# Kernel optimization log

Hardware: AMD Instinct MI355X
Metric: run time of the kernel (lower is better)

## Reference

```python
import jax, jax.numpy as jnp
import numpy as np

D_MODEL = 1024; D_STATE = 64; D_CONV = 7; EXPAND = 2; HEADDIM = 64; NGROUPS = 1
D_INNER = EXPAND * D_MODEL            # 2048
NHEADS = D_INNER // HEADDIM           # 32
D_IN_PROJ = 2 * D_INNER + 2 * (2 * NGROUPS * D_STATE) + 2 * NHEADS  # 4416
CONV_DIM = D_INNER + 2 * (2 * NGROUPS * D_STATE)                     # 2304
BATCH = 2; SEQLEN = 2048
EPS = 1e-5


def setup_inputs() -> dict:
    key = jax.random.key(0)
    ks = jax.random.split(key, 8)
    u = jax.random.normal(ks[0], (BATCH, SEQLEN, D_MODEL), jnp.float32)
    W_in = jax.random.normal(ks[1], (D_IN_PROJ, D_MODEL), jnp.float32) * 0.02
    conv_w = jax.random.normal(ks[2], (CONV_DIM, 1, D_CONV), jnp.float32) * 0.2
    conv_b = jax.random.normal(ks[3], (CONV_DIM,), jnp.float32) * 0.02
    # dt_bias init as in module: inv-softplus of dt sampled log-uniform in [dt_min, dt_max]
    dt = jnp.exp(jax.random.uniform(ks[4], (NHEADS,)) * (np.log(0.1) - np.log(0.001)) + np.log(0.001))
    dt = jnp.clip(dt, 1e-4)
    dt_bias = dt + jnp.log(-jnp.expm1(-dt))
    A_log = jnp.zeros((NHEADS,), jnp.float32)          # A = -exp(A_log) = -1
    Dp = jnp.ones((NHEADS,), jnp.float32)
    fc_D_w = jax.random.normal(ks[5], (NHEADS, D_INNER), jnp.float32) * 0.02
    norm_w = jnp.ones((D_INNER,), jnp.float32)
    W_out = jax.random.normal(ks[6], (D_MODEL, D_INNER), jnp.float32) * 0.02
    return dict(u=u, W_in=W_in, conv_w=conv_w, conv_b=conv_b, dt_bias=dt_bias,
                A_log=A_log, Dp=Dp, fc_D_w=fc_D_w, norm_w=norm_w, W_out=W_out)


def reference(u, W_in, conv_w, conv_b, dt_bias, A_log, Dp, fc_D_w, norm_w, W_out):
    b, L, _ = u.shape
    gn = NGROUPS * D_STATE
    zxbcdt = jnp.einsum('bld,ed->ble', u, W_in)              # (b,L,4416)
    A = -jnp.exp(A_log)                                       # (H,)
    z = zxbcdt[..., :D_INNER]
    xBC = zxbcdt[..., D_INNER:D_INNER + CONV_DIM]
    dt_raw = zxbcdt[..., D_INNER + CONV_DIM:]                 # (b,L,2H)
    # fwd dt + time-flipped bwd dt stacked along batch -> (2b,L,H)
    dt = jnp.concatenate([dt_raw[..., :NHEADS], dt_raw[..., NHEADS:][:, ::-1]], axis=0)
    dt = jax.nn.softplus(dt + dt_bias)                        # dt_limit=(0,inf): softplus already >= 0
    # depthwise conv1d, 'same' padding
    xc = jnp.transpose(xBC, (0, 2, 1))                        # (b,Cd,L)
    xc = jax.lax.conv_general_dilated(xc, conv_w, (1,), [(D_CONV // 2, D_CONV // 2)],
                                      dimension_numbers=('NCH', 'OIH', 'NCH'),
                                      feature_group_count=CONV_DIM)
    xc = xc + conv_b[None, :, None]
    xBC = jax.nn.silu(jnp.transpose(xc, (0, 2, 1)))           # (b,L,Cd)
    x = xBC[..., :D_INNER]
    BC = xBC[..., D_INNER:]
    x_og = x
    x2 = jnp.concatenate([x, x[:, ::-1]], axis=0)             # (2b,L,d_inner)
    BC2 = jnp.concatenate([BC[..., :2 * gn], BC[..., 2 * gn:][:, ::-1]], axis=0)
    Bm = BC2[..., :gn].reshape(2 * b, L, NGROUPS, D_STATE)
    Cm = BC2[..., gn:].reshape(2 * b, L, NGROUPS, D_STATE)
    x_scan = x2.reshape(2 * b, L, NHEADS, HEADDIM)
    hpg = NHEADS // NGROUPS
    Bh = jnp.repeat(Bm, hpg, axis=2)                          # (2b,L,H,N)
    Ch = jnp.repeat(Cm, hpg, axis=2)

    def step(state, ins):                                     # state: (2b,H,P,N)
        x_t, dt_t, B_t, C_t = ins
        ex = jnp.exp(A[None, :, None, None] * dt_t[:, :, None, None])
        state = state * ex + x_t[..., None] * B_t[:, :, None, :]
        y_t = jnp.sum(state * C_t[:, :, None, :], axis=-1)    # (2b,H,P)
        return state, y_t

    xs = (jnp.moveaxis(x_scan, 1, 0), jnp.moveaxis(dt, 1, 0),
          jnp.moveaxis(Bh, 1, 0), jnp.moveaxis(Ch, 1, 0))
    state0 = jnp.zeros((2 * b, NHEADS, HEADDIM, D_STATE), u.dtype)
    _, ys = jax.lax.scan(step, state0, xs)                    # (L,2b,H,P)
    y = jnp.moveaxis(ys, 0, 1).reshape(2 * b, L, D_INNER)
    # shift_right: drop last step, zero at t=0
    y = jnp.concatenate([jnp.zeros_like(y[:, :1]), y[:, :-1]], axis=1)
    y_fw, y_bw = y[:b], y[b:][:, ::-1]
    diag_heads = jnp.einsum('bld,hd->blh', x_og, fc_D_w) + Dp # fc_D(x_og) with bias D
    diag = jnp.repeat(diag_heads, HEADDIM, axis=-1)           # expand per-head -> d_inner
    y = y_fw + y_bw + x_og * diag
    # RMSNormGated (norm before gate)
    rms = jnp.sqrt(jnp.mean(y * y, axis=-1, keepdims=True) + EPS)
    y = norm_w * (y / rms) * jax.nn.silu(z)
    return jnp.einsum('ble,de->bld', y, W_out)
```

## Files before the change

kernel.cpp:

```cpp
#include <hip/hip_runtime.h>
#include <cstdint>
#include <cstddef>

#define L_SEQ   2048
#define DMODEL  1024
#define DINNER  2048
#define NHEADS_ 32
#define HEADDIM_ 64
#define DSTATE  64
#define CONVDIM 2304
#define DINPROJ 4416
#define DINPROJ_P 4480
#define BATCH_  2
#define EPS_    1e-5f
#define PITCH   72
#define KSPL    8

typedef __attribute__((ext_vector_type(8))) short bf16x8;
typedef __attribute__((ext_vector_type(4))) float f32x4;
typedef unsigned short ushort_t;
typedef unsigned int uint_t;
typedef __attribute__((address_space(3))) unsigned int as3_uint;
typedef __attribute__((address_space(1))) const unsigned int as1_uint;

__device__ __forceinline__ float silu_f(float v) { return v / (1.f + __expf(-v)); }
__device__ __forceinline__ ushort_t f2bf(float f) {
    uint_t u = __float_as_uint(f);
    return (ushort_t)((u + 0x7FFFu + ((u >> 16) & 1u)) >> 16);
}
__device__ __forceinline__ float bf2f(ushort_t u) {
    return __uint_as_float(((uint_t)u) << 16);
}
__device__ __forceinline__ void gload16(const void* g, void* l) {
    __builtin_amdgcn_global_load_lds((as1_uint*)g, (as3_uint*)l, 16, 0, 0);
}

#define N0U ((size_t)(4096 * 1024 / 4))
#define N1U ((size_t)(DINPROJ_P * DMODEL / 4))
#define N2U ((size_t)(DMODEL * DINNER / 4))
#define N3U ((size_t)(64 * DINNER / 4))
__global__ __launch_bounds__(256)
void cvt_all(const float* __restrict__ u, const float* __restrict__ W_in,
             const float* __restrict__ W_out, const float* __restrict__ fcD,
             ushort_t* __restrict__ ubf, ushort_t* __restrict__ wibf,
             ushort_t* __restrict__ wobf, ushort_t* __restrict__ fcdbf) {
    size_t unit = (size_t)blockIdx.x * 256 + threadIdx.x;
    const float* src; ushort_t* dst; size_t i4; bool zero = false;
    if (unit < N0U) {
        i4 = unit; src = u; dst = ubf;
    } else if (unit < N0U + N1U) {
        i4 = unit - N0U; src = W_in; dst = wibf;
        zero = ((int)(i4 / (DMODEL / 4)) >= DINPROJ);
    } else if (unit < N0U + N1U + N2U) {
        i4 = unit - N0U - N1U; src = W_out; dst = wobf;
    } else {
        i4 = unit - N0U - N1U - N2U; src = fcD; dst = fcdbf;
        zero = ((int)(i4 / (DINNER / 4)) >= NHEADS_);
    }
    float4 v = zero ? make_float4(0.f, 0.f, 0.f, 0.f)
                    : reinterpret_cast<const float4*>(src)[i4];
    ushort_t* d = dst + i4 * 4;
    d[0] = f2bf(v.x); d[1] = f2bf(v.y); d[2] = f2bf(v.z); d[3] = f2bf(v.w);
}

template<int BM, int BN, int WGM, int WGN, int FM, int FN, int MODE>
__global__ __launch_bounds__(256)
void gemm_nt_mfma(const ushort_t* __restrict__ A, const ushort_t* __restrict__ B,
                  float* __restrict__ C, ushort_t* __restrict__ Cbf,
                  int M, int N, int K, int lda, int ldb, int nbn) {
    const int nwg = gridDim.x;
    const int orig = blockIdx.x;
    const int xcd = orig & 7, q = nwg >> 3, r = nwg & 7;
    const int wg = ((xcd < r) ? (xcd * (q + 1)) : (r * (q + 1) + (xcd - r) * q)) + (orig >> 3);

    int bm, bn, kbeg, kend, ks = 0;
    if (MODE == 2) {
        bm = (wg / nbn) * BM; bn = 0; ks = wg % nbn;
        kbeg = ks * (K / nbn); kend = kbeg + K / nbn;
    } else {
        bm = (wg / nbn) * BM; bn = (wg % nbn) * BN;
        kbeg = 0; kend = K;
    }

    constexpr int BUFSZ = (BM + BN) * 64;
    constexpr int EPI_B = (MODE == 2) ? 0 : BM * 256;
    constexpr int SMEM_B = (2 * BUFSZ > EPI_B) ? 2 * BUFSZ : EPI_B;
    __shared__ __align__(16) char smem[SMEM_B];

    const int tid = threadIdx.x;
    const int wave = tid >> 6, lane = tid & 63;
    const int wr = wave / WGN, wc = wave % WGN;
    const int fr = lane & 15, kg = lane >> 4;

    constexpr int AI = BM / 64, BI = BN / 64;
    size_t aoff[AI]; int aLds[AI];
#pragma unroll
    for (int pp = 0; pp < AI; ++pp) {
        int p = wave * AI + pp;
        int row = p * 16 + (lane >> 2);
        int c16 = (lane & 3) ^ ((row >> 1) & 3);
        aoff[pp] = (size_t)(bm + row) * lda + c16 * 8;
        aLds[pp] = p * 1024;
    }
    size_t boff[BI]; int bLds[BI];
#pragma unroll
    for (int pp = 0; pp < BI; ++pp) {
        int p = wave * BI + pp;
        int row = p * 16 + (lane >> 2);
        int c16 = (lane & 3) ^ ((row >> 1) & 3);
        boff[pp] = (size_t)(bn + row) * ldb + c16 * 8;
        bLds[pp] = BM * 64 + p * 1024;
    }

    auto stage = [&](int buf, int k0) {
        char* bp = smem + buf * BUFSZ;
#pragma unroll
        for (int pp = 0; pp < AI; ++pp) gload16(&A[aoff[pp] + k0], bp + aLds[pp]);
#pragma unroll
        for (int pp = 0; pp < BI; ++pp) gload16(&B[boff[pp] + k0], bp + bLds[pp]);
    };

    f32x4 acc[FM][FN];
#pragma unroll
    for (int m = 0; m < FM; ++m)
#pragma unroll
        for (int n = 0; n < FN; ++n) acc[m][n] = (f32x4){0.f, 0.f, 0.f, 0.f};

    stage(0, kbeg);
    __syncthreads();

    const int NT = (kend - kbeg) / 32;
    for (int t = 0; t < NT; ++t) {
        const int cur = t & 1;
        if (t + 1 < NT) stage(cur ^ 1, kbeg + (t + 1) * 32);

        const char* bp = smem + cur * BUFSZ;
        bf16x8 af[FM], bfv[FN];
#pragma unroll
        for (int m = 0; m < FM; ++m) {
            int row = wr * FM * 16 + m * 16 + fr;
            af[m] = *reinterpret_cast<const bf16x8*>(bp + row * 64 + ((kg ^ ((row >> 1) & 3)) << 4));
        }
#pragma unroll
        for (int n = 0; n < FN; ++n) {
            int row = wc * FN * 16 + n * 16 + fr;
            bfv[n] = *reinterpret_cast<const bf16x8*>(bp + BM * 64 + row * 64 + ((kg ^ ((row >> 1) & 3)) << 4));
        }
#pragma unroll
        for (int m = 0; m < FM; ++m)
#pragma unroll
            for (int n = 0; n < FN; ++n)
                acc[m][n] = __builtin_amdgcn_mfma_f32_16x16x32_bf16(af[m], bfv[n], acc[m][n], 0, 0, 0);
        __syncthreads();
    }

    const int rg = lane >> 4;
    if (MODE == 2) {
        float* Cp = C + (size_t)ks * M * NHEADS_;
#pragma unroll
        for (int m = 0; m < FM; ++m)
#pragma unroll
            for (int n = 0; n < FN; ++n) {
                int col = wc * FN * 16 + n * 16 + fr;
#pragma unroll
                for (int r = 0; r < 4; ++r) {
                    int rowg = bm + wr * FM * 16 + m * 16 + rg * 4 + r;
                    if (col < NHEADS_) Cp[(size_t)rowg * NHEADS_ + col] = acc[m][n][r];
                }
            }
    } else {
        constexpr int ESZ = (MODE == 1) ? 2 : 4;
        char* ct = smem;
#pragma unroll
        for (int m = 0; m < FM; ++m)
#pragma unroll
            for (int n = 0; n < FN; ++n) {
#pragma unroll
                for (int r = 0; r < 4; ++r) {
                    int lr = wr * FM * 16 + m * 16 + rg * 4 + r;
                    int lc = wc * FN * 16 + n * 16 + fr;
                    int byte = (lr * 256 + lc * ESZ) ^ ((lr & 7) << 4);
                    if (MODE == 1) *reinterpret_cast<ushort_t*>(ct + byte) = f2bf(acc[m][n][r]);
                    else           *reinterpret_cast<float*>(ct + byte) = acc[m][n][r];
                }
            }
        __syncthreads();
        const int lrow = tid >> 4, seg16 = (tid & 15) * 16;
#pragma unroll
        for (int j = 0; j < BM / 16; ++j) {
            int lr = j * 16 + lrow;
            uint4 v = *reinterpret_cast<const uint4*>(ct + ((lr * 256 + seg16) ^ ((lr & 7) << 4)));
            if (MODE == 1)
                *reinterpret_cast<uint4*>(&Cbf[(size_t)(bm + lr) * N + bn + seg16 / 2]) = v;
            else
                *reinterpret_cast<uint4*>(&C[(size_t)(bm + lr) * N + bn + seg16 / 4]) = v;
        }
    }
}

__global__ __launch_bounds__(256)
void conv_kernel(const ushort_t* __restrict__ zxbf, const float* __restrict__ conv_w,
                 const float* __restrict__ conv_b, ushort_t* __restrict__ xBCbf) {
    const int c = blockIdx.x * 256 + threadIdx.x;
    const int t0 = blockIdx.y * 16;
    const int beta = blockIdx.z;
    float w[7];
#pragma unroll
    for (int k = 0; k < 7; ++k) w[k] = conv_w[c * 7 + k];
    const float bias = conv_b[c];
    const ushort_t* in = zxbf + (size_t)beta * L_SEQ * DINPROJ_P + DINNER + c;
    float win[7];
#pragma unroll
    for (int j = 0; j < 6; ++j) {
        int t = t0 - 3 + j;
        win[j] = (t >= 0 && t < L_SEQ) ? bf2f(in[(size_t)t * DINPROJ_P]) : 0.f;
    }
    for (int i = 0; i < 16; ++i) {
        int t = t0 + i;
        int tl = t + 3;
        win[6] = (tl < L_SEQ) ? bf2f(in[(size_t)tl * DINPROJ_P]) : 0.f;
        float acc = bias;
#pragma unroll
        for (int k = 0; k < 7; ++k) acc += win[k] * w[k];
        xBCbf[((size_t)beta * L_SEQ + t) * CONVDIM + c] = f2bf(silu_f(acc));
#pragma unroll
        for (int j = 0; j < 6; ++j) win[j] = win[j + 1];
    }
}

__global__ __launch_bounds__(256)
void dtla_kernel(const ushort_t* __restrict__ zxbf, const float* __restrict__ dt_bias,
                 const float* __restrict__ A_log, float* __restrict__ labuf) {
    const int idx = blockIdx.x * 256 + threadIdx.x;
    const int h   = idx & 31;
    const int tau = (idx >> 5) & (L_SEQ - 1);
    const int bd  = idx >> 16;
    const int dir = bd >> 1, beta = bd & 1;
    const int tt  = dir ? (L_SEQ - 1 - tau) : tau;
    const float dtraw = bf2f(zxbf[((size_t)beta * L_SEQ + tt) * DINPROJ_P + DINNER + CONVDIM + dir * NHEADS_ + h]);
    const float Ah = -__expf(A_log[h]);
    const float dtv = dtraw + dt_bias[h];
    const float sp = (dtv > 15.f) ? dtv : log1pf(__expf(dtv));
    labuf[((size_t)bd * NHEADS_ + h) * L_SEQ + tau] = Ah * sp;
}

__global__ __launch_bounds__(256)
void ssd_chunk_kernel(const ushort_t* __restrict__ xBCbf, const float* __restrict__ labuf,
                      float* __restrict__ Pbuf, ushort_t* __restrict__ sdel,
                      ushort_t* __restrict__ yfw, ushort_t* __restrict__ ybw) {
    const int c  = blockIdx.x;
    const int h  = blockIdx.y;
    const int bd = blockIdx.z;
    const int dir = bd >> 1, beta = bd & 1;
    const int tid = threadIdx.x;
    const int wave = tid >> 6, lane = tid & 63;
    const int wr = wave >> 1, wc = wave & 1;
    const int fr = lane & 15, kg = lane >> 4, rg = lane >> 4;

    __shared__ short Bs[64 * PITCH], Cs[64 * PITCH], XTs[64 * PITCH],
                     BTs[64 * PITCH], Ms[64 * PITCH];
    __shared__ float lslds[64];

    const int row = tid >> 2, seg = tid & 3;
    const int tau_r = c * 64 + row;
    const int tt = dir ? (L_SEQ - 1 - tau_r) : tau_r;
    const ushort_t* gbase = xBCbf + ((size_t)beta * L_SEQ + tt) * CONVDIM;

    union U4 { uint4 v; ushort_t s[8]; };
    U4 x0, x1, b0, b1, c0, c1;
    x0.v = *reinterpret_cast<const uint4*>(gbase + h * 64 + seg * 16);
    x1.v = *reinterpret_cast<const uint4*>(gbase + h * 64 + seg * 16 + 8);
    b0.v = *reinterpret_cast<const uint4*>(gbase + DINNER + dir * 128 + seg * 16);
    b1.v = *reinterpret_cast<const uint4*>(gbase + DINNER + dir * 128 + seg * 16 + 8);
    c0.v = *reinterpret_cast<const uint4*>(gbase + DINNER + dir * 128 + 64 + seg * 16);
    c1.v = *reinterpret_cast<const uint4*>(gbase + DINNER + dir * 128 + 64 + seg * 16 + 8);

    *reinterpret_cast<uint4*>(&Bs[row * PITCH + seg * 16])     = b0.v;
    *reinterpret_cast<uint4*>(&Bs[row * PITCH + seg * 16 + 8]) = b1.v;
    *reinterpret_cast<uint4*>(&Cs[row * PITCH + seg * 16])     = c0.v;
    *reinterpret_cast<uint4*>(&Cs[row * PITCH + seg * 16 + 8]) = c1.v;
#pragma unroll
    for (int k = 0; k < 8; ++k) {
        XTs[(seg * 16 + k) * PITCH + row]     = x0.s[k];
        XTs[(seg * 16 + 8 + k) * PITCH + row] = x1.s[k];
    }

    if (tid < 64) {
        float v = labuf[((size_t)bd * NHEADS_ + h) * L_SEQ + c * 64 + tid];
#pragma unroll
        for (int d = 1; d < 64; d <<= 1) {
            float t = __shfl_up(v, d);
            if (lane >= d) v += t;
        }
        lslds[tid] = v;
        Pbuf[((size_t)bd * NHEADS_ + h) * L_SEQ + c * 64 + tid] = __expf(v);
    }
    __syncthreads();

    {
        const float wrow = __expf(lslds[63] - lslds[row]);
#pragma unroll
        for (int k = 0; k < 8; ++k) {
            BTs[(seg * 16 + k) * PITCH + row]     = (short)f2bf(bf2f(b0.s[k]) * wrow);
            BTs[(seg * 16 + 8 + k) * PITCH + row] = (short)f2bf(bf2f(b1.s[k]) * wrow);
        }
    }

    f32x4 accg[2][2];
#pragma unroll
    for (int mi = 0; mi < 2; ++mi)
#pragma unroll
        for (int nj = 0; nj < 2; ++nj) accg[mi][nj] = (f32x4){0.f, 0.f, 0.f, 0.f};
#pragma unroll
    for (int s = 0; s < 2; ++s) {
        int koff = kg * 8 + s * 32;
        bf16x8 af[2], bfv[2];
#pragma unroll
        for (int mi = 0; mi < 2; ++mi)
            af[mi] = *reinterpret_cast<const bf16x8*>(&Cs[(wr * 32 + mi * 16 + fr) * PITCH + koff]);
#pragma unroll
        for (int nj = 0; nj < 2; ++nj)
            bfv[nj] = *reinterpret_cast<const bf16x8*>(&Bs[(wc * 32 + nj * 16 + fr) * PITCH + koff]);
#pragma unroll
        for (int mi = 0; mi < 2; ++mi)
#pragma unroll
            for (int nj = 0; nj < 2; ++nj)
                accg[mi][nj] = __builtin_amdgcn_mfma_f32_16x16x32_bf16(af[mi], bfv[nj], accg[mi][nj], 0, 0, 0);
    }

#pragma unroll
    for (int mi = 0; mi < 2; ++mi)
#pragma unroll
        for (int nj = 0; nj < 2; ++nj) {
            int j = wc * 32 + nj * 16 + fr;
            float lsj = lslds[j];
#pragma unroll
            for (int r = 0; r < 4; ++r) {
                int i = wr * 32 + mi * 16 + rg * 4 + r;
                float v = accg[mi][nj][r];
                v = (i >= j) ? v * __expf(lslds[i] - lsj) : 0.f;
                Ms[i * PITCH + j] = (short)f2bf(v);
            }
        }
    __syncthreads();

    f32x4 accy[2][2], accs[2][2];
#pragma unroll
    for (int mi = 0; mi < 2; ++mi)
#pragma unroll
        for (int nj = 0; nj < 2; ++nj) {
            accy[mi][nj] = (f32x4){0.f, 0.f, 0.f, 0.f};
            accs[mi][nj] = (f32x4){0.f, 0.f, 0.f, 0.f};
        }
#pragma unroll
    for (int s = 0; s < 2; ++s) {
        int koff = kg * 8 + s * 32;
        bf16x8 am[2], axt[2], bxt[2], bbt[2];
#pragma unroll
        for (int mi = 0; mi < 2; ++mi) {
            am[mi]  = *reinterpret_cast<const bf16x8*>(&Ms[(wr * 32 + mi * 16 + fr) * PITCH + koff]);
            axt[mi] = *reinterpret_cast<const bf16x8*>(&XTs[(wr * 32 + mi * 16 + fr) * PITCH + koff]);
        }
#pragma unroll
        for (int nj = 0; nj < 2; ++nj) {
            bxt[nj] = *reinterpret_cast<const bf16x8*>(&XTs[(wc * 32 + nj * 16 + fr) * PITCH + koff]);
            bbt[nj] = *reinterpret_cast<const bf16x8*>(&BTs[(wc * 32 + nj * 16 + fr) * PITCH + koff]);
        }
#pragma unroll
        for (int mi = 0; mi < 2; ++mi)
#pragma unroll
            for (int nj = 0; nj < 2; ++nj) {
                accy[mi][nj] = __builtin_amdgcn_mfma_f32_16x16x32_bf16(am[mi], bxt[nj], accy[mi][nj], 0, 0, 0);
                accs[mi][nj] = __builtin_amdgcn_mfma_f32_16x16x32_bf16(axt[mi], bbt[nj], accs[mi][nj], 0, 0, 0);
            }
    }

    ushort_t* Yt = (ushort_t*)Bs;
    ushort_t* St = (ushort_t*)Cs;
#pragma unroll
    for (int mi = 0; mi < 2; ++mi)
#pragma unroll
        for (int nj = 0; nj < 2; ++nj) {
#pragma unroll
            for (int r = 0; r < 4; ++r) {
                int i  = wr * 32 + mi * 16 + rg * 4 + r;
                int jd = wc * 32 + nj * 16 + fr;
                St[i * 64 + jd] = f2bf(accs[mi][nj][r]);
                Yt[i * 64 + jd] = f2bf(accy[mi][nj][r]);
            }
        }
    __syncthreads();

    ushort_t* yout = dir ? ybw : yfw;
    ushort_t* sdp = sdel + (((size_t)bd * NHEADS_ + h) * 32 + c) * 4096;
    for (int un = tid; un < 512; un += 256) {
        const int rowi = un >> 3, ch = un & 7;
        uint4 sv = *reinterpret_cast<const uint4*>(St + rowi * 64 + ch * 8);
        *reinterpret_cast<uint4*>(sdp + rowi * 64 + ch * 8) = sv;
        uint4 yv = *reinterpret_cast<const uint4*>(Yt + rowi * 64 + ch * 8);
        int tau = c * 64 + rowi;
        int tout;
        if (tau == L_SEQ - 1) { tout = dir ? (L_SEQ - 1) : 0; yv = make_uint4(0, 0, 0, 0); }
        else                  { tout = dir ? (L_SEQ - 2 - tau) : (tau + 1); }
        *reinterpret_cast<uint4*>(yout + ((size_t)beta * L_SEQ + tout) * DINNER + h * 64 + ch * 8) = yv;
    }
}

__global__ __launch_bounds__(256)
void ssd_scan_kernel(const float* __restrict__ Pbuf, ushort_t* __restrict__ sdel) {
    const int bh = blockIdx.x;
    const int qt = blockIdx.y;
    const int eo = qt * 1024 + threadIdx.x * 4;
    ushort_t* base = sdel + (size_t)bh * 32 * 4096;
    const float* Pb = Pbuf + (size_t)bh * L_SEQ;

    float S0 = 0.f, S1 = 0.f, S2 = 0.f, S3 = 0.f;
    uint2 d = *reinterpret_cast<const uint2*>(base + eo);
    for (int c = 0; c < 32; ++c) {
        uint2 dn;
        if (c + 1 < 32) dn = *reinterpret_cast<const uint2*>(base + (size_t)(c + 1) * 4096 + eo);
        const float ptot = Pb[c * 64 + 63];
        uint2 pv;
        pv.x = (uint_t)f2bf(S0) | ((uint_t)f2bf(S1) << 16);
        pv.y = (uint_t)f2bf(S2) | ((uint_t)f2bf(S3) << 16);
        *reinterpret_cast<uint2*>(base + (size_t)c * 4096 + eo) = pv;
        S0 = ptot * S0 + bf2f((ushort_t)(d.x & 0xFFFF));
        S1 = ptot * S1 + bf2f((ushort_t)(d.x >> 16));
        S2 = ptot * S2 + bf2f((ushort_t)(d.y & 0xFFFF));
        S3 = ptot * S3 + bf2f((ushort_t)(d.y >> 16));
        d = dn;
    }
}

__global__ __launch_bounds__(256)
void ssd_yinter_kernel(const ushort_t* __restrict__ xBCbf, const float* __restrict__ Pbuf,
                       const ushort_t* __restrict__ sin_buf,
                       ushort_t* __restrict__ yfw, ushort_t* __restrict__ ybw) {
    const int c  = blockIdx.x;
    const int h  = blockIdx.y;
    const int bd = blockIdx.z;
    const int dir = bd >> 1, beta = bd & 1;
    const int tid = threadIdx.x;
    const int wave = tid >> 6, lane = tid & 63;
    const int fr = lane & 15, kg = lane >> 4, rg = lane >> 4;
    const int i0 = wave * 16;

    __shared__ short Cs[64 * PITCH], Ss[64 * PITCH];
    __shared__ float Pl[64];

    const int row = tid >> 2, seg = tid & 3;
    {
        const int tau_r = c * 64 + row;
        const int tt = dir ? (L_SEQ - 1 - tau_r) : tau_r;
        const ushort_t* gbase = xBCbf + ((size_t)beta * L_SEQ + tt) * CONVDIM + DINNER + dir * 128 + 64;
        uint4 cv0 = *reinterpret_cast<const uint4*>(gbase + seg * 16);
        uint4 cv1 = *reinterpret_cast<const uint4*>(gbase + seg * 16 + 8);
        *reinterpret_cast<uint4*>(&Cs[row * PITCH + seg * 16])     = cv0;
        *reinterpret_cast<uint4*>(&Cs[row * PITCH + seg * 16 + 8]) = cv1;
    }
    {
        const ushort_t* sb = sin_buf + (((size_t)bd * NHEADS_ + h) * 32 + c) * 4096;
        for (int un = tid; un < 512; un += 256) {
            const int ri = un >> 3, ch = un & 7;
            uint4 v = *reinterpret_cast<const uint4*>(sb + ri * 64 + ch * 8);
            *reinterpret_cast<uint4*>(&Ss[ri * PITCH + ch * 8]) = v;
        }
    }
    if (tid < 64) Pl[tid] = Pbuf[((size_t)bd * NHEADS_ + h) * L_SEQ + c * 64 + tid];
    __syncthreads();

    f32x4 accy[4];
#pragma unroll
    for (int nf = 0; nf < 4; ++nf) accy[nf] = (f32x4){0.f, 0.f, 0.f, 0.f};
#pragma unroll
    for (int s = 0; s < 2; ++s) {
        int koff = kg * 8 + s * 32;
        bf16x8 af = *reinterpret_cast<const bf16x8*>(&Cs[(i0 + fr) * PITCH + koff]);
#pragma unroll
        for (int nf = 0; nf < 4; ++nf) {
            bf16x8 bfv = *reinterpret_cast<const bf16x8*>(&Ss[(nf * 16 + fr) * PITCH + koff]);
            accy[nf] = __builtin_amdgcn_mfma_f32_16x16x32_bf16(af, bfv, accy[nf], 0, 0, 0);
        }
    }
    __syncthreads();

    ushort_t* Yt = (ushort_t*)Cs;
#pragma unroll
    for (int nf = 0; nf < 4; ++nf) {
        int hdl = nf * 16 + fr;
#pragma unroll
        for (int r = 0; r < 4; ++r) {
            int i = i0 + rg * 4 + r;
            Yt[i * 64 + hdl] = f2bf(accy[nf][r] * Pl[i]);
        }
    }
    __syncthreads();

    ushort_t* yout = dir ? ybw : yfw;
    for (int un = tid; un < 512; un += 256) {
        const int ri = un >> 3, ch = un & 7;
        int tau = c * 64 + ri;
        if (tau == L_SEQ - 1) continue;
        int tout = dir ? (L_SEQ - 2 - tau) : (tau + 1);
        ushort_t* gp = yout + ((size_t)beta * L_SEQ + tout) * DINNER + h * 64 + ch * 8;
        union U4 { uint4 v; ushort_t s[8]; } yo, cv, res;
        yo.v = *reinterpret_cast<const uint4*>(gp);
        cv.v = *reinterpret_cast<const uint4*>(Yt + ri * 64 + ch * 8);
#pragma unroll
        for (int k = 0; k < 8; ++k) res.s[k] = f2bf(bf2f(yo.s[k]) + bf2f(cv.s[k]));
        *reinterpret_cast<uint4*>(gp) = res.v;
    }
}

__global__ __launch_bounds__(256)
void combine_rms(const ushort_t* __restrict__ yfw, const ushort_t* __restrict__ ybw,
                 const ushort_t* __restrict__ xBCbf, const float* __restrict__ dpart,
                 const float* __restrict__ Dp,
                 const ushort_t* __restrict__ zxbf, const float* __restrict__ norm_w,
                 ushort_t* __restrict__ ybf) {
    const int row = blockIdx.x;
    const int tid = threadIdx.x;
    union U4 { uint4 v; ushort_t s[8]; };
    U4 yf, yb, xv, zv;
    yf.v = *reinterpret_cast<const uint4*>(yfw + (size_t)row * DINNER + tid * 8);
    yb.v = *reinterpret_cast<const uint4*>(ybw + (size_t)row * DINNER + tid * 8);
    xv.v = *reinterpret_cast<const uint4*>(xBCbf + (size_t)row * CONVDIM + tid * 8);
    zv.v = *reinterpret_cast<const uint4*>(zxbf + (size_t)row * DINPROJ_P + tid * 8);
    const int hh = tid >> 3;
    float dgv = Dp[hh];
#pragma unroll
    for (int ks = 0; ks < KSPL; ++ks)
        dgv += dpart[((size_t)ks * (BATCH_ * L_SEQ) + row) * NHEADS_ + hh];
    float v[8];
    float ss = 0.f;
#pragma unroll
    for (int i = 0; i < 8; ++i) {
        float val = bf2f(yf.s[i]) + bf2f(yb.s[i]) + bf2f(xv.s[i]) * dgv;
        v[i] = val;
        ss += val * val;
    }
    ss += __shfl_xor(ss, 1);  ss += __shfl_xor(ss, 2);  ss += __shfl_xor(ss, 4);
    ss += __shfl_xor(ss, 8);  ss += __shfl_xor(ss, 16); ss += __shfl_xor(ss, 32);
    __shared__ float wsum[4];
    if ((tid & 63) == 0) wsum[tid >> 6] = ss;
    __syncthreads();
    ss = wsum[0] + wsum[1] + wsum[2] + wsum[3];
    const float inv = rsqrtf(ss * (1.f / DINNER) + EPS_);
    U4 outv;
#pragma unroll
    for (int i = 0; i < 8; ++i) {
        int c = tid * 8 + i;
        outv.s[i] = f2bf(norm_w[c] * v[i] * inv * silu_f(bf2f(zv.s[i])));
    }
    *reinterpret_cast<uint4*>(ybf + (size_t)row * DINNER + tid * 8) = outv.v;
}

extern "C" void kernel_launch(void* const* d_in, const int* in_sizes, int n_in,
                              void* d_out, int out_size, void* d_ws, size_t ws_size,
                              hipStream_t stream) {
    const float* u       = (const float*)d_in[0];
    const float* W_in    = (const float*)d_in[1];
    const float* conv_w  = (const float*)d_in[2];
    const float* conv_b  = (const float*)d_in[3];
    const float* dt_bias = (const float*)d_in[4];
    const float* A_log   = (const float*)d_in[5];
    const float* Dp      = (const float*)d_in[6];
    const float* fc_D_w  = (const float*)d_in[7];
    const float* norm_w  = (const float*)d_in[8];
    const float* W_out   = (const float*)d_in[9];
    float* out = (float*)d_out;

    const int ROWS = BATCH_ * L_SEQ;
    ushort_t* zxbf  = (ushort_t*)d_ws;
    ushort_t* xBCbf = zxbf  + (size_t)ROWS * DINPROJ_P;
    ushort_t* yfw   = xBCbf + (size_t)ROWS * CONVDIM;
    ushort_t* ybw   = yfw   + (size_t)ROWS * DINNER;
    float* dpart = (float*)(ybw + (size_t)ROWS * DINNER);
    float* labuf = dpart + (size_t)KSPL * ROWS * NHEADS_;
    float* Pbuf  = labuf + (size_t)4 * NHEADS_ * L_SEQ;
    ushort_t* sdel = (ushort_t*)(Pbuf + (size_t)4 * NHEADS_ * L_SEQ);
    ushort_t* wobf = sdel + (size_t)4 * NHEADS_ * 32 * 64 * 64;
    ushort_t* fcdbf = wobf + (size_t)DMODEL * DINNER;
    ushort_t* ubf  = fcdbf + (size_t)64 * DINNER;
    ushort_t* wibf = ubf  + (size_t)ROWS * DMODEL;
    ushort_t* ybf  = ubf;

    const size_t total_units = N0U + N1U + N2U + N3U;
    cvt_all<<<(int)((total_units + 255) / 256), 256, 0, stream>>>(
        u, W_in, W_out, fc_D_w, ubf, wibf, wobf, fcdbf);

    gemm_nt_mfma<128, 128, 2, 2, 4, 4, 1><<<(ROWS / 128) * (DINPROJ_P / 128), 256, 0, stream>>>(
        ubf, wibf, nullptr, zxbf, ROWS, DINPROJ_P, DMODEL, DMODEL, DMODEL, DINPROJ_P / 128);

    dim3 gc(CONVDIM / 256, L_SEQ / 16, BATCH_);
    conv_kernel<<<gc, 256, 0, stream>>>(zxbf, conv_w, conv_b, xBCbf);

    dtla_kernel<<<(4 * L_SEQ * NHEADS_) / 256, 256, 0, stream>>>(zxbf, dt_bias, A_log, labuf);

    dim3 ga(32, NHEADS_, 4);
    ssd_chunk_kernel<<<ga, 256, 0, stream>>>(xBCbf, labuf, Pbuf, sdel, yfw, ybw);

    dim3 gsn(4 * NHEADS_, 4);
    ssd_scan_kernel<<<gsn, 256, 0, stream>>>(Pbuf, sdel);

    dim3 gy(32, NHEADS_, 4);
    ssd_yinter_kernel<<<gy, 256, 0, stream>>>(xBCbf, Pbuf, sdel, yfw, ybw);

    gemm_nt_mfma<64, 64, 2, 2, 2, 2, 2><<<(ROWS / 64) * KSPL, 256, 0, stream>>>(
        xBCbf, fcdbf, dpart, nullptr, ROWS, 64, DINNER, CONVDIM, DINNER, KSPL);

    combine_rms<<<ROWS, 256, 0, stream>>>(yfw, ybw, xBCbf, dpart, Dp, zxbf, norm_w, ybf);

    gemm_nt_mfma<128, 64, 2, 2, 4, 2, 0><<<(ROWS / 128) * (DMODEL / 64), 256, 0, stream>>>(
        ybf, wobf, out, nullptr, ROWS, DMODEL, DINNER, DINNER, DINNER, DMODEL / 64);
}
```

Measured before the change: 207.3 us.

## Replace in-projection GEMM with 256x256-tile 8-wave phased MFMA kernel

Measured after the change: 219.6 us. +5.9%, slower.

```diff
diff --git a/kernel.cpp b/kernel.cpp
--- a/kernel.cpp
+++ b/kernel.cpp
@@ -10,7 +10,7 @@
 #define DSTATE  64
 #define CONVDIM 2304
 #define DINPROJ 4416
-#define DINPROJ_P 4480
+#define DINPROJ_P 4608
 #define BATCH_  2
 #define EPS_    1e-5f
 #define PITCH   72
@@ -45,6 +45,7 @@
              ushort_t* __restrict__ ubf, ushort_t* __restrict__ wibf,
              ushort_t* __restrict__ wobf, ushort_t* __restrict__ fcdbf) {
     size_t unit = (size_t)blockIdx.x * 256 + threadIdx.x;
+    if (unit >= N0U + N1U + N2U + N3U) return;
     const float* src; ushort_t* dst; size_t i4; bool zero = false;
     if (unit < N0U) {
         i4 = unit; src = u; dst = ubf;
@@ -63,6 +64,137 @@
     d[0] = f2bf(v.x); d[1] = f2bf(v.y); d[2] = f2bf(v.z); d[3] = f2bf(v.w);
 }
 
+__global__ __launch_bounds__(512, 2)
+void gemm_8ph(const ushort_t* __restrict__ Ap, const ushort_t* __restrict__ Bp,
+              ushort_t* __restrict__ Cbf, int M, int N, int K, int nbn) {
+    const int nwg = gridDim.x;
+    const int orig = blockIdx.x;
+    const int xcd = orig & 7, q_ = nwg >> 3, r_ = nwg & 7;
+    const int wg = ((xcd < r_) ? (xcd * (q_ + 1)) : (r_ * (q_ + 1) + (xcd - r_) * q_)) + (orig >> 3);
+    const int bm = (wg / nbn) * 256, bn = (wg % nbn) * 256;
+
+    __shared__ __align__(16) char smem[131072];
+
+    const int tid = threadIdx.x;
+    const int wave = tid >> 6, lane = tid & 63;
+    const int wr = wave >> 2, wc = wave & 3;
+    const int fr = lane & 15, kg = lane >> 4, rg = lane >> 4;
+
+    const ushort_t* gptr[8]; uint_t glds[8];
+#pragma unroll
+    for (int i = 0; i < 8; ++i) {
+        int unit = i >> 1, g = i & 1;
+        int isB = unit & 1, half = unit >> 1;
+        int rbase = half * 128 + wave * 16 + g * 8;
+        int rl = rbase + (lane >> 3);
+        int slot = (lane & 7) ^ (lane >> 3);
+        gptr[i] = (isB ? Bp : Ap) + (size_t)((isB ? bn : bm) + rl) * (size_t)K + slot * 8;
+        glds[i] = (uint_t)(isB * 32768 + rbase * 128);
+    }
+    auto stage = [&](int pbuf, int t) {
+#pragma unroll
+        for (int i = 0; i < 8; ++i)
+            gload16(gptr[i] + (size_t)t * 64, smem + pbuf * 65536 + glds[i]);
+    };
+
+    f32x4 acc[8][4];
+#pragma unroll
+    for (int m = 0; m < 8; ++m)
+#pragma unroll
+        for (int n = 0; n < 4; ++n) acc[m][n] = (f32x4){0.f, 0.f, 0.f, 0.f};
+
+    bf16x8 aF[4][2];
+    bf16x8 bF[2][2][2];
+
+    auto lda_frag = [&](int pbuf, int mh) {
+#pragma unroll
+        for (int mm = 0; mm < 4; ++mm)
+#pragma unroll
+            for (int kk = 0; kk < 2; ++kk) {
+                int Rl = wr * 128 + mh * 64 + mm * 16 + fr;
+                aF[mm][kk] = *reinterpret_cast<const bf16x8*>(
+                    smem + pbuf * 65536 + Rl * 128 + (((kk * 4 + kg) ^ (Rl & 7)) << 4));
+            }
+    };
+    auto ldb_frag = [&](int pbuf, int nh) {
+#pragma unroll
+        for (int nn = 0; nn < 2; ++nn)
+#pragma unroll
+            for (int kk = 0; kk < 2; ++kk) {
+                int Rl = wc * 64 + (nh * 2 + nn) * 16 + fr;
+                bF[nh][nn][kk] = *reinterpret_cast<const bf16x8*>(
+                    smem + pbuf * 65536 + 32768 + Rl * 128 + (((kk * 4 + kg) ^ (Rl & 7)) << 4));
+            }
+    };
+    auto do_mfma = [&](int mh, int nh) {
+        __builtin_amdgcn_s_setprio(1);
+#pragma unroll
+        for (int mm = 0; mm < 4; ++mm)
+#pragma unroll
+            for (int nn = 0; nn < 2; ++nn)
+#pragma unroll
+                for (int kk = 0; kk < 2; ++kk)
+                    acc[mh * 4 + mm][nh * 2 + nn] = __builtin_amdgcn_mfma_f32_16x16x32_bf16(
+                        aF[mm][kk], bF[nh][nn][kk], acc[mh * 4 + mm][nh * 2 + nn], 0, 0, 0);
+        __builtin_amdgcn_s_setprio(0);
+    };
+
+    const int NT = K / 64;
+    stage(0, 0);
+    asm volatile("s_waitcnt vmcnt(0)" ::: "memory");
+    __builtin_amdgcn_sched_barrier(0);
+    __builtin_amdgcn_s_barrier();
+
+    for (int t = 0; t < NT; ++t) {
+        const int p = t & 1;
+        if (t + 1 < NT) stage(p ^ 1, t + 1);
+        if (t > 0) {
+            if (t + 1 < NT) asm volatile("s_waitcnt vmcnt(8)" ::: "memory");
+            else            asm volatile("s_waitcnt vmcnt(0)" ::: "memory");
+            __builtin_amdgcn_sched_barrier(0);
+        }
+        __builtin_amdgcn_s_barrier();
+        lda_frag(p, 0); ldb_frag(p, 0);
+        asm volatile("s_waitcnt lgkmcnt(0)" ::: "memory");
+        __builtin_amdgcn_sched_barrier(0);
+        do_mfma(0, 0);
+        __builtin_amdgcn_s_barrier();
+        ldb_frag(p, 1);
+        asm volatile("s_waitcnt lgkmcnt(0)" ::: "memory");
+        __builtin_amdgcn_sched_barrier(0);
+        do_mfma(0, 1);
+        __builtin_amdgcn_s_barrier();
+        lda_frag(p, 1);
+        asm volatile("s_waitcnt lgkmcnt(0)" ::: "memory");
+        __builtin_amdgcn_sched_barrier(0);
+        do_mfma(1, 0);
+        __builtin_amdgcn_s_barrier();
+        do_mfma(1, 1);
+        __builtin_amdgcn_s_barrier();
+    }
+
+    char* ct = smem;
+#pragma unroll
+    for (int m = 0; m < 8; ++m)
+#pragma unroll
+        for (int n = 0; n < 4; ++n) {
+#pragma unroll
+            for (int r = 0; r < 4; ++r) {
+                int lr = wr * 128 + m * 16 + rg * 4 + r;
+                int lc = wc * 64 + n * 16 + fr;
+                int byte = lr * 512 + ((lc * 2) ^ ((lr & 7) << 4));
+                *reinterpret_cast<ushort_t*>(ct + byte) = f2bf(acc[m][n][r]);
+            }
+        }
+    __syncthreads();
+    for (int pass = 0; pass < 16; ++pass) {
+        int unit = pass * 512 + tid;
+        int row = unit >> 5, u = unit & 31;
+        uint4 v = *reinterpret_cast<const uint4*>(ct + row * 512 + ((u * 16) ^ ((row & 7) << 4)));
+        *reinterpret_cast<uint4*>(&Cbf[(size_t)(bm + row) * N + bn + u * 8]) = v;
+    }
+}
+
 template<int BM, int BN, int WGM, int WGN, int FM, int FN, int MODE>
 __global__ __launch_bounds__(256)
 void gemm_nt_mfma(const ushort_t* __restrict__ A, const ushort_t* __restrict__ B,
@@ -169,7 +301,6 @@
                 }
             }
     } else {
-        constexpr int ESZ = (MODE == 1) ? 2 : 4;
         char* ct = smem;
 #pragma unroll
         for (int m = 0; m < FM; ++m)
@@ -179,9 +310,8 @@
                 for (int r = 0; r < 4; ++r) {
                     int lr = wr * FM * 16 + m * 16 + rg * 4 + r;
                     int lc = wc * FN * 16 + n * 16 + fr;
-                    int byte = (lr * 256 + lc * ESZ) ^ ((lr & 7) << 4);
-                    if (MODE == 1) *reinterpret_cast<ushort_t*>(ct + byte) = f2bf(acc[m][n][r]);
-                    else           *reinterpret_cast<float*>(ct + byte) = acc[m][n][r];
+                    int byte = (lr * 256 + lc * 4) ^ ((lr & 7) << 4);
+                    *reinterpret_cast<float*>(ct + byte) = acc[m][n][r];
                 }
             }
         __syncthreads();
@@ -190,10 +320,7 @@
         for (int j = 0; j < BM / 16; ++j) {
             int lr = j * 16 + lrow;
             uint4 v = *reinterpret_cast<const uint4*>(ct + ((lr * 256 + seg16) ^ ((lr & 7) << 4)));
-            if (MODE == 1)
-                *reinterpret_cast<uint4*>(&Cbf[(size_t)(bm + lr) * N + bn + seg16 / 2]) = v;
-            else
-                *reinterpret_cast<uint4*>(&C[(size_t)(bm + lr) * N + bn + seg16 / 4]) = v;
+            *reinterpret_cast<uint4*>(&C[(size_t)(bm + lr) * N + bn + seg16 / 4]) = v;
         }
     }
 }
@@ -589,8 +716,8 @@
     cvt_all<<<(int)((total_units + 255) / 256), 256, 0, stream>>>(
         u, W_in, W_out, fc_D_w, ubf, wibf, wobf, fcdbf);
 
-    gemm_nt_mfma<128, 128, 2, 2, 4, 4, 1><<<(ROWS / 128) * (DINPROJ_P / 128), 256, 0, stream>>>(
-        ubf, wibf, nullptr, zxbf, ROWS, DINPROJ_P, DMODEL, DMODEL, DMODEL, DINPROJ_P / 128);
+    gemm_8ph<<<(ROWS / 256) * (DINPROJ_P / 256), 512, 0, stream>>>(
+        ubf, wibf, zxbf, ROWS, DINPROJ_P, DMODEL, DINPROJ_P / 256);
 
     dim3 gc(CONVDIM / 256, L_SEQ / 16, BATCH_);
     conv_kernel<<<gc, 256, 0, stream>>>(zxbf, conv_w, conv_b, xBCbf);
```
